# Kernel tuning notes

Measured on AMD Instinct MI355X. Metric: run time of the kernel, lower is better.

The kernel has to match this reference:

```python
import jax, jax.numpy as jnp
import numpy as np

B, H, W, C = 32, 64, 64, 64
F = 128
KH = KW = 3
SH = SW = 1
P = KH * KW * C  # flattened patch size = 576


def _glorot(key, shape):
    fan_in = KH * KW * C
    fan_out = KH * KW * F
    limit = np.sqrt(6.0 / (fan_in + fan_out)).astype(np.float32)
    return jax.random.uniform(key, shape, jnp.float32, -limit, limit)


def setup_inputs() -> dict:
    key = jax.random.key(0)
    k1, k2, k3 = jax.random.split(key, 3)
    inputs = jax.random.normal(k1, (B, H, W, C), dtype=jnp.float32)
    kernel = _glorot(k2, (KH, KW, C, F))
    control_points = _glorot(k3, (KH, KW, C, F))
    bias = jnp.zeros((F,), dtype=jnp.float32)
    return {"inputs": inputs, "kernel": kernel, "bias": bias, "control_points": control_points}


def _extract_patches(x):
    # SAME padding, stride 1; TF extract_patches ordering: (kh, kw, C), C fastest
    xp = jnp.pad(x, ((0, 0), (1, 1), (1, 1), (0, 0)))
    patches = jnp.stack(
        [xp[:, i:i + H, j:j + W, :] for i in range(KH) for j in range(KW)],
        axis=3,
    )  # [B, H, W, KH*KW, C]
    return patches.reshape(B, H, W, P)


def reference(inputs, kernel, bias, control_points):
    conv_out = jax.lax.conv_general_dilated(
        inputs, kernel, (SH, SW), "SAME",
        dimension_numbers=("NHWC", "HWIO", "NHWC"),
    )  # [B, H, W, F]

    # RBF branch via ||a-b||^2 = ||a||^2 + ||b||^2 - 2 a.b
    p = _extract_patches(inputs).reshape(-1, P)        # [N, P]
    c = control_points.reshape(P, F)                   # [P, F]
    pn = jnp.sum(p * p, axis=1, keepdims=True)         # [N, 1]
    cn = jnp.sum(c * c, axis=0)                        # [F]
    d = pn + cn - 2.0 * (p @ c)                        # [N, F] squared distances
    gamma = 1.0 / (2.0 * jnp.mean(d))                  # global mean over all patches/filters
    kan = jnp.exp(-gamma * d).reshape(B, H, W, F)

    return conv_out + kan + bias
```

## Files before the change

kernel.cpp:

```cpp
#include <hip/hip_runtime.h>


#define B_ 32
#define H_ 64
#define W_ 64
#define C_ 64
#define F_ 128
#define P_ 576
#define NPIX (B_*H_*W_)
#define NF   (NPIX*F_)

typedef __bf16  bf16x8 __attribute__((ext_vector_type(8)));
typedef float   f32x4  __attribute__((ext_vector_type(4)));

union BFU { __bf16 h; ushort s; };
union PKU { __bf16 h[2]; uint u; };

__device__ __forceinline__ ushort f2bf(float f) { BFU q; q.h = (__bf16)f; return q.s; }
__device__ __forceinline__ uint pk(float a, float b) {
    PKU q; q.h[0] = (__bf16)a; q.h[1] = (__bf16)b; return q.u;
}

__global__ void k_prep(const float* __restrict__ wgt, const float* __restrict__ ctrl,
                       ushort* __restrict__ wsB, float* __restrict__ cn,
                       float* __restrict__ accum, float* __restrict__ tab) {
    __shared__ __attribute__((aligned(16))) float sh[1024];
    const int t = threadIdx.x;

    if (blockIdx.x < 288) {
        int e = blockIdx.x * 256 + t;
        int p = e >> 7, f = e & 127;
        int kc = p >> 6, r = p & 63;
        int ks = r >> 5, quad = (r >> 3) & 3, j = r & 7;
        int ntg = f >> 4, l16 = f & 15;
        int off0 = (kc * 2 + ks) * 8192 + ntg * 512 + (quad * 16 + l16) * 8 + j;
        wsB[off0]        = f2bf(wgt[e]);
        wsB[off0 + 4096] = f2bf(ctrl[e]);
        return;
    }
    if (blockIdx.x == 288) {
        int col = t & 31, pc8 = t >> 5;
        f32x4 a = {0.f, 0.f, 0.f, 0.f};
        const float* base = ctrl + col * 4;
        #pragma unroll 4
        for (int p = pc8 * 72; p < pc8 * 72 + 72; ++p) {
            f32x4 v = *(const f32x4*)(base + p * F_);
            a += v * v;
        }
        f32x4* sh4 = (f32x4*)sh;
        sh4[t] = a;
        __syncthreads();
        f32x4 s = {0.f, 0.f, 0.f, 0.f};
        if (t < 32) {
            #pragma unroll
            for (int q = 0; q < 8; ++q) s += sh4[q * 32 + t];
            *(f32x4*)(cn + t * 4) = s;
        }
        float tot = s.x + s.y + s.z + s.w;
        if (t < 64) {
            #pragma unroll
            for (int off = 32; off >= 1; off >>= 1) tot += __shfl_down(tot, off, 64);
            if (t == 0) accum[0] = tot;
        }
        return;
    }

    for (int e = t; e < 576; e += 256) {
        const f32x4* row = (const f32x4*)(ctrl + e * F_);
        f32x4 a = {0.f, 0.f, 0.f, 0.f};
        #pragma unroll 8
        for (int q = 0; q < 32; ++q) a += row[q];
        sh[e] = a.x + a.y + a.z + a.w;
    }
    __syncthreads();
    for (int idx = t; idx < 576; idx += 256) {
        int q = idx >> 6, c = idx & 63;
        int ry = q / 3, rx = q - 3 * ry;
        int my = (ry == 0) ? 3 : (ry == 2) ? 6 : 7;
        int mx = (rx == 0) ? 3 : (rx == 2) ? 6 : 7;
        float s = 0.f;
        #pragma unroll
        for (int ki = 0; ki < 3; ++ki)
            #pragma unroll
            for (int kj = 0; kj < 3; ++kj)
                if ((my >> ki & 1) && (mx >> kj & 1))
                    s += sh[(ki * 3 + kj) * 64 + c];
        tab[idx] = s;
    }
}

__launch_bounds__(256)
__global__ void k_gamma(const float* __restrict__ in, const float* __restrict__ tab,
                        float* __restrict__ spn, float* __restrict__ spc) {
    __shared__ float shs[4], shp[4];
    const int t = threadIdx.x, seg = t & 15, grp = t >> 4;
    float s = 0.f, pc = 0.f;
    #pragma unroll 4
    for (int it = 0; it < 16; ++it) {
        int pix = blockIdx.x * 256 + it * 16 + grp;
        int y = (pix >> 6) & 63, x = pix & 63;
        float4 v = *((const float4*)(in + pix * 64) + seg);
        int ry = (y == 0) ? 0 : (y == 63) ? 2 : 1;
        int rx = (x == 0) ? 0 : (x == 63) ? 2 : 1;
        float4 tv = *((const float4*)(tab + (ry * 3 + rx) * 64) + seg);
        float wq = (float)((3 - (y == 0) - (y == 63)) * (3 - (x == 0) - (x == 63)));
        s  += wq * (v.x*v.x + v.y*v.y + v.z*v.z + v.w*v.w);
        pc += v.x*tv.x + v.y*tv.y + v.z*tv.z + v.w*tv.w;
    }
    #pragma unroll
    for (int off = 32; off >= 1; off >>= 1) {
        s  += __shfl_down(s,  off, 64);
        pc += __shfl_down(pc, off, 64);
    }
    if ((t & 63) == 0) { shs[t >> 6] = s; shp[t >> 6] = pc; }
    __syncthreads();
    if (t == 0)  spn[blockIdx.x] = shs[0] + shs[1] + shs[2] + shs[3];
    if (t == 64) spc[blockIdx.x] = shp[0] + shp[1] + shp[2] + shp[3];
}

__launch_bounds__(512, 4)
__global__ void k_main(const float* __restrict__ in, const ushort* __restrict__ wsB,
                       const float* __restrict__ bias, const float* __restrict__ cn,
                       const float* __restrict__ accum, const float* __restrict__ spn,
                       const float* __restrict__ spc, float* __restrict__ out) {
    __shared__ __attribute__((aligned(16))) ushort smem[18208];
    ushort* lI   = smem;
    float*  sArr = (float*)(smem + 17408);
    float*  pnAr = (float*)(smem + 17952);

    const int tid = threadIdx.x;
    const int n0  = blockIdx.x * 128;
    const int b   = n0 >> 12;
    const int y0  = (n0 >> 6) & 63;
    const float* inb = in + b * 262144;

    const int w     = tid >> 6, lane = tid & 63;
    const int fq    = w & 3, mhalf = w >> 2;
    const int quad  = lane >> 4, l16 = lane & 15;
    const int fq2   = fq * 2;

    const uint4* bp = (const uint4*)wsB + fq2 * 64 + lane;

    uint4 cw0 = bp[0],   cw1 = bp[64];
    uint4 cc0 = bp[512], cc1 = bp[576];

    for (int g = tid; g < 2176; g += 512) {
        int row4 = g / 544;
        int rem  = g - row4 * 544;
        int px = rem >> 3, c = rem & 7;
        int y = y0 + row4 - 1, x = px - 1;
        float4 v0 = make_float4(0.f, 0.f, 0.f, 0.f), v1 = v0;
        if (y >= 0 && y < 64 && x >= 0 && x < 64) {
            const float* sp = inb + y * 4096 + x * 64 + c * 8;
            v0 = *(const float4*)sp;
            v1 = *(const float4*)(sp + 4);
        }
        uint4 o = { pk(v0.x, v0.y), pk(v0.z, v0.w), pk(v1.x, v1.y), pk(v1.z, v1.w) };
        *(uint4*)&lI[(row4 * 68 + px) * 64 + ((c ^ (px & 7)) << 3)] = o;
        float s8 = v0.x*v0.x + v0.y*v0.y + v0.z*v0.z + v0.w*v0.w
                 + v1.x*v1.x + v1.y*v1.y + v1.z*v1.z + v1.w*v1.w;
        s8 += __shfl_xor(s8, 1, 64);
        s8 += __shfl_xor(s8, 2, 64);
        s8 += __shfl_xor(s8, 4, 64);
        if ((g & 7) == 0) sArr[row4 * 68 + px] = s8;
    }
    __syncthreads();

    if (tid < 128) {
        int yr = tid >> 6, x = tid & 63;
        float a = 0.f;
        #pragma unroll
        for (int dr = 0; dr < 3; ++dr)
            #pragma unroll
            for (int dc = 0; dc < 3; ++dc)
                a += sArr[(yr + dr) * 68 + x + dc];
        pnAr[tid] = a;
    }
    __syncthreads();

    f32x4 accW[4][2], accC[4][2];
    #pragma unroll
    for (int mt = 0; mt < 4; ++mt)
        #pragma unroll
        for (int nt = 0; nt < 2; ++nt) {
            accW[mt][nt] = (f32x4){0.f, 0.f, 0.f, 0.f};
            accC[mt][nt] = (f32x4){0.f, 0.f, 0.f, 0.f};
        }

    #pragma unroll 1
    for (int t18 = 0; t18 < 18; ++t18) {
        const int kc = t18 >> 1, ks = t18 & 1;
        const int ki = (kc >= 6) ? 2 : (kc >= 3) ? 1 : 0;
        const int kj = kc - 3 * ki;

        uint4 nw0, nw1, nc0, nc1;
        if (t18 < 17) {
            const uint4* np = bp + (t18 + 1) * 1024;
            nw0 = np[0];   nw1 = np[64];
            nc0 = np[512]; nc1 = np[576];
        }

        bf16x8 bw[2], bc[2];
        bw[0] = __builtin_bit_cast(bf16x8, cw0);
        bw[1] = __builtin_bit_cast(bf16x8, cw1);
        bc[0] = __builtin_bit_cast(bf16x8, cc0);
        bc[1] = __builtin_bit_cast(bf16x8, cc1);

        const int swk = (l16 + kj) & 7;
        const int rb0 = (mhalf + ki) * 68 + l16 + kj;
        const int sw  = ((ks * 4 + quad) ^ swk) << 3;
        #pragma unroll
        for (int mt = 0; mt < 4; ++mt) {
            bf16x8 a = *(const bf16x8*)&lI[(rb0 + mt * 16) * 64 + sw];
            #pragma unroll
            for (int nt = 0; nt < 2; ++nt) {
                accW[mt][nt] = __builtin_amdgcn_mfma_f32_16x16x32_bf16(a, bw[nt], accW[mt][nt], 0, 0, 0);
                accC[mt][nt] = __builtin_amdgcn_mfma_f32_16x16x32_bf16(a, bc[nt], accC[mt][nt], 0, 0, 0);
            }
        }
        cw0 = nw0; cw1 = nw1; cc0 = nc0; cc1 = nc1;
    }

    float sp = 0.f, sc = 0.f;
    #pragma unroll
    for (int q = 0; q < 8; ++q) {
        sp += spn[q * 64 + lane];
        sc += spc[q * 64 + lane];
    }
    #pragma unroll
    for (int off = 32; off >= 1; off >>= 1) {
        sp += __shfl_xor(sp, off, 64);
        sc += __shfl_xor(sc, off, 64);
    }
    float Sd = 128.f * sp + 131072.f * accum[0] - 2.f * sc;
    float g  = 0.5f * 16777216.f / Sd;
    float bv[2], cv[2];
    #pragma unroll
    for (int nt = 0; nt < 2; ++nt) {
        int gf = fq * 32 + nt * 16 + l16;
        bv[nt] = bias[gf];
        cv[nt] = cn[gf];
    }
    #pragma unroll
    for (int mt = 0; mt < 4; ++mt) {
        int rloc = mhalf * 64 + mt * 16 + quad * 4;
        float pv[4];
        #pragma unroll
        for (int r = 0; r < 4; ++r) pv[r] = pnAr[rloc + r];
        int gm = n0 + rloc;
        #pragma unroll
        for (int nt = 0; nt < 2; ++nt) {
            int gf = fq * 32 + nt * 16 + l16;
            #pragma unroll
            for (int r = 0; r < 4; ++r) {
                float d = pv[r] + cv[nt] - 2.f * accC[mt][nt][r];
                out[(gm + r) * F_ + gf] = accW[mt][nt][r] + bv[nt] + __expf(-g * d);
            }
        }
    }
}

extern "C" void kernel_launch(void* const* d_in, const int* in_sizes, int n_in,
                              void* d_out, int out_size, void* d_ws, size_t ws_size,
                              hipStream_t stream) {
    const float* in   = (const float*)d_in[0];
    const float* wgt  = (const float*)d_in[1];
    const float* bias = (const float*)d_in[2];
    const float* ctrl = (const float*)d_in[3];
    float* out = (float*)d_out;

    char* ws = (char*)d_ws;
    ushort* wsB   = (ushort*)(ws + 0);
    float*  cn    = (float*) (ws + 294912);
    float*  accum = (float*) (ws + 295424);
    float*  tab   = (float*) (ws + 295488);
    float*  spn   = (float*) (ws + 297792);
    float*  spc   = (float*) (ws + 299840);

    k_prep  <<<290,        256, 0, stream>>>(wgt, ctrl, wsB, cn, accum, tab);
    k_gamma <<<NPIX / 256, 256, 0, stream>>>(in, tab, spn, spc);
    k_main  <<<NPIX / 128, 512, 0, stream>>>(in, wsB, bias, cn, accum, spn, spc, out);
}
```

Before: 142.2 us.

## Shrink main tile to one image row and merge gamma reduction into prep

Each main-kernel block now handles one image row (64 pixels) with 256 threads instead of two rows with 512. This doubles the grid and cuts LDS per block, but also lowers halo reuse, since 3 input rows are loaded per output row instead of 4 per 2. The per-pixel gamma partial-sum work moves into the prep kernel's extra blocks, and the control-point table becomes its own tiny single-block kernel. The launch count stays at three, but the gamma reduction now runs concurrently with weight packing.

New measurement: 151.6 us. 1.07x slower.

```diff
diff --git a/kernel.cpp b/kernel.cpp
--- a/kernel.cpp
+++ b/kernel.cpp
@@ -21,10 +21,40 @@
     PKU q; q.h[0] = (__bf16)a; q.h[1] = (__bf16)b; return q.u;
 }
 
-__global__ void k_prep(const float* __restrict__ wgt, const float* __restrict__ ctrl,
+__global__ void k_tab(const float* __restrict__ ctrl, float* __restrict__ tab) {
+    __shared__ float sh[576];
+    const int t = threadIdx.x;
+    for (int e = t; e < 576; e += 256) {
+        const f32x4* row = (const f32x4*)(ctrl + e * F_);
+        f32x4 a = {0.f, 0.f, 0.f, 0.f};
+        #pragma unroll 8
+        for (int q = 0; q < 32; ++q) a += row[q];
+        sh[e] = a.x + a.y + a.z + a.w;
+    }
+    __syncthreads();
+    for (int idx = t; idx < 576; idx += 256) {
+        int q = idx >> 6, c = idx & 63;
+        int ry = q / 3, rx = q - 3 * ry;
+        int my = (ry == 0) ? 3 : (ry == 2) ? 6 : 7;
+        int mx = (rx == 0) ? 3 : (rx == 2) ? 6 : 7;
+        float s = 0.f;
+        #pragma unroll
+        for (int ki = 0; ki < 3; ++ki)
+            #pragma unroll
+            for (int kj = 0; kj < 3; ++kj)
+                if ((my >> ki & 1) && (mx >> kj & 1))
+                    s += sh[(ki * 3 + kj) * 64 + c];
+        tab[idx] = s;
+    }
+}
+
+__global__ void k_prep(const float* __restrict__ in, const float* __restrict__ wgt,
+                       const float* __restrict__ ctrl, const float* __restrict__ tab,
                        ushort* __restrict__ wsB, float* __restrict__ cn,
-                       float* __restrict__ accum, float* __restrict__ tab) {
+                       float* __restrict__ accum, float* __restrict__ spn,
+                       float* __restrict__ spc) {
     __shared__ __attribute__((aligned(16))) float sh[1024];
+    __shared__ float shs[4], shp[4];
     const int t = threadIdx.x;
 
     if (blockIdx.x < 288) {
@@ -65,39 +95,12 @@
         return;
     }
 
-    for (int e = t; e < 576; e += 256) {
-        const f32x4* row = (const f32x4*)(ctrl + e * F_);
-        f32x4 a = {0.f, 0.f, 0.f, 0.f};
-        #pragma unroll 8
-        for (int q = 0; q < 32; ++q) a += row[q];
-        sh[e] = a.x + a.y + a.z + a.w;
-    }
-    __syncthreads();
-    for (int idx = t; idx < 576; idx += 256) {
-        int q = idx >> 6, c = idx & 63;
-        int ry = q / 3, rx = q - 3 * ry;
-        int my = (ry == 0) ? 3 : (ry == 2) ? 6 : 7;
-        int mx = (rx == 0) ? 3 : (rx == 2) ? 6 : 7;
-        float s = 0.f;
-        #pragma unroll
-        for (int ki = 0; ki < 3; ++ki)
-            #pragma unroll
-            for (int kj = 0; kj < 3; ++kj)
-                if ((my >> ki & 1) && (mx >> kj & 1))
-                    s += sh[(ki * 3 + kj) * 64 + c];
-        tab[idx] = s;
-    }
-}
-
-__launch_bounds__(256)
-__global__ void k_gamma(const float* __restrict__ in, const float* __restrict__ tab,
-                        float* __restrict__ spn, float* __restrict__ spc) {
-    __shared__ float shs[4], shp[4];
-    const int t = threadIdx.x, seg = t & 15, grp = t >> 4;
+    const int sb = blockIdx.x - 289;
+    const int seg = t & 15, grp = t >> 4;
     float s = 0.f, pc = 0.f;
     #pragma unroll 4
     for (int it = 0; it < 16; ++it) {
-        int pix = blockIdx.x * 256 + it * 16 + grp;
+        int pix = sb * 256 + it * 16 + grp;
         int y = (pix >> 6) & 63, x = pix & 63;
         float4 v = *((const float4*)(in + pix * 64) + seg);
         int ry = (y == 0) ? 0 : (y == 63) ? 2 : 1;
@@ -114,28 +117,27 @@
     }
     if ((t & 63) == 0) { shs[t >> 6] = s; shp[t >> 6] = pc; }
     __syncthreads();
-    if (t == 0)  spn[blockIdx.x] = shs[0] + shs[1] + shs[2] + shs[3];
-    if (t == 64) spc[blockIdx.x] = shp[0] + shp[1] + shp[2] + shp[3];
-}
-
-__launch_bounds__(512, 4)
+    if (t == 0)  spn[sb] = shs[0] + shs[1] + shs[2] + shs[3];
+    if (t == 64) spc[sb] = shp[0] + shp[1] + shp[2] + shp[3];
+}
+
+__launch_bounds__(256, 4)
 __global__ void k_main(const float* __restrict__ in, const ushort* __restrict__ wsB,
                        const float* __restrict__ bias, const float* __restrict__ cn,
                        const float* __restrict__ accum, const float* __restrict__ spn,
                        const float* __restrict__ spc, float* __restrict__ out) {
-    __shared__ __attribute__((aligned(16))) ushort smem[18208];
+    __shared__ __attribute__((aligned(16))) ushort smem[13600];
     ushort* lI   = smem;
-    float*  sArr = (float*)(smem + 17408);
-    float*  pnAr = (float*)(smem + 17952);
+    float*  sArr = (float*)(smem + 13056);
+    float*  pnAr = (float*)(smem + 13464);
 
     const int tid = threadIdx.x;
-    const int n0  = blockIdx.x * 128;
+    const int n0  = blockIdx.x * 64;
     const int b   = n0 >> 12;
     const int y0  = (n0 >> 6) & 63;
     const float* inb = in + b * 262144;
 
-    const int w     = tid >> 6, lane = tid & 63;
-    const int fq    = w & 3, mhalf = w >> 2;
+    const int fq    = tid >> 6, lane = tid & 63;
     const int quad  = lane >> 4, l16 = lane & 15;
     const int fq2   = fq * 2;
 
@@ -144,11 +146,11 @@
     uint4 cw0 = bp[0],   cw1 = bp[64];
     uint4 cc0 = bp[512], cc1 = bp[576];
 
-    for (int g = tid; g < 2176; g += 512) {
-        int row4 = g / 544;
-        int rem  = g - row4 * 544;
+    for (int g = tid; g < 1632; g += 256) {
+        int row3 = g / 544;
+        int rem  = g - row3 * 544;
         int px = rem >> 3, c = rem & 7;
-        int y = y0 + row4 - 1, x = px - 1;
+        int y = y0 + row3 - 1, x = px - 1;
         float4 v0 = make_float4(0.f, 0.f, 0.f, 0.f), v1 = v0;
         if (y >= 0 && y < 64 && x >= 0 && x < 64) {
             const float* sp = inb + y * 4096 + x * 64 + c * 8;
@@ -156,24 +158,23 @@
             v1 = *(const float4*)(sp + 4);
         }
         uint4 o = { pk(v0.x, v0.y), pk(v0.z, v0.w), pk(v1.x, v1.y), pk(v1.z, v1.w) };
-        *(uint4*)&lI[(row4 * 68 + px) * 64 + ((c ^ (px & 7)) << 3)] = o;
+        *(uint4*)&lI[(row3 * 68 + px) * 64 + ((c ^ (px & 7)) << 3)] = o;
         float s8 = v0.x*v0.x + v0.y*v0.y + v0.z*v0.z + v0.w*v0.w
                  + v1.x*v1.x + v1.y*v1.y + v1.z*v1.z + v1.w*v1.w;
         s8 += __shfl_xor(s8, 1, 64);
         s8 += __shfl_xor(s8, 2, 64);
         s8 += __shfl_xor(s8, 4, 64);
-        if ((g & 7) == 0) sArr[row4 * 68 + px] = s8;
-    }
-    __syncthreads();
-
-    if (tid < 128) {
-        int yr = tid >> 6, x = tid & 63;
+        if ((g & 7) == 0) sArr[row3 * 68 + px] = s8;
+    }
+    __syncthreads();
+
+    if (tid < 64) {
         float a = 0.f;
         #pragma unroll
         for (int dr = 0; dr < 3; ++dr)
             #pragma unroll
             for (int dc = 0; dc < 3; ++dc)
-                a += sArr[(yr + dr) * 68 + x + dc];
+                a += sArr[dr * 68 + tid + dc];
         pnAr[tid] = a;
     }
     __syncthreads();
@@ -207,7 +208,7 @@
         bc[1] = __builtin_bit_cast(bf16x8, cc1);
 
         const int swk = (l16 + kj) & 7;
-        const int rb0 = (mhalf + ki) * 68 + l16 + kj;
+        const int rb0 = ki * 68 + l16 + kj;
         const int sw  = ((ks * 4 + quad) ^ swk) << 3;
         #pragma unroll
         for (int mt = 0; mt < 4; ++mt) {
@@ -243,7 +244,7 @@
     }
     #pragma unroll
     for (int mt = 0; mt < 4; ++mt) {
-        int rloc = mhalf * 64 + mt * 16 + quad * 4;
+        int rloc = mt * 16 + quad * 4;
         float pv[4];
         #pragma unroll
         for (int r = 0; r < 4; ++r) pv[r] = pnAr[rloc + r];
@@ -277,7 +278,7 @@
     float*  spn   = (float*) (ws + 297792);
     float*  spc   = (float*) (ws + 299840);
 
-    k_prep  <<<290,        256, 0, stream>>>(wgt, ctrl, wsB, cn, accum, tab);
-    k_gamma <<<NPIX / 256, 256, 0, stream>>>(in, tab, spn, spc);
-    k_main  <<<NPIX / 128, 512, 0, stream>>>(in, wsB, bias, cn, accum, spn, spc, out);
-}
+    k_tab  <<<1,         256, 0, stream>>>(ctrl, tab);
+    k_prep <<<801,       256, 0, stream>>>(in, wgt, ctrl, tab, wsB, cn, accum, spn, spc);
+    k_main <<<NPIX / 64, 256, 0, stream>>>(in, wsB, bias, cn, accum, spn, spc, out);
+}
```

## Pre-convert input to padded swizzled bf16 image and stage via global_load_lds

Applied to the files above, without the earlier changes.

k_gamma now also writes a bf16, row-padded, XOR-swizzled copy of the input plus per-pixel squared norms into workspace. k_main loads its halo tile straight into LDS with global_load_lds, skipping per-block fp32 loads, conversion and duplicate halo reads. Patch norms come from a 3x3 box sum of the per-pixel norms. This adds an extra 17 MB write/read pass through the workspace, and a fallback kernel covers the case where the workspace is too small.

Result: slower. 153.9 us (+8.2%).

```diff
diff --git a/kernel.cpp b/kernel.cpp
--- a/kernel.cpp
+++ b/kernel.cpp
@@ -21,9 +21,15 @@
     PKU q; q.h[0] = (__bf16)a; q.h[1] = (__bf16)b; return q.u;
 }
 
+__device__ __forceinline__ void gll16(const void* g, void* l) {
+    __builtin_amdgcn_global_load_lds((const __attribute__((address_space(1))) void*)g,
+                                     (__attribute__((address_space(3))) void*)l, 16, 0, 0);
+}
+
 __global__ void k_prep(const float* __restrict__ wgt, const float* __restrict__ ctrl,
                        ushort* __restrict__ wsB, float* __restrict__ cn,
-                       float* __restrict__ accum, float* __restrict__ tab) {
+                       float* __restrict__ accum, float* __restrict__ tab,
+                       uint4* __restrict__ zeroblk) {
     __shared__ __attribute__((aligned(16))) float sh[1024];
     const int t = threadIdx.x;
 
@@ -39,6 +45,7 @@
         return;
     }
     if (blockIdx.x == 288) {
+        if (t < 8) zeroblk[t] = (uint4){0u, 0u, 0u, 0u};
         int col = t & 31, pc8 = t >> 5;
         f32x4 a = {0.f, 0.f, 0.f, 0.f};
         const float* base = ctrl + col * 4;
@@ -91,9 +98,12 @@
 
 __launch_bounds__(256)
 __global__ void k_gamma(const float* __restrict__ in, const float* __restrict__ tab,
-                        float* __restrict__ spn, float* __restrict__ spc) {
+                        float* __restrict__ spn, float* __restrict__ spc,
+                        ushort* __restrict__ imgbf, float* __restrict__ sG,
+                        int wimg) {
     __shared__ float shs[4], shp[4];
     const int t = threadIdx.x, seg = t & 15, grp = t >> 4;
+    const int cc = seg >> 1, half = seg & 1;
     float s = 0.f, pc = 0.f;
     #pragma unroll 4
     for (int it = 0; it < 16; ++it) {
@@ -104,8 +114,28 @@
         int rx = (x == 0) ? 0 : (x == 63) ? 2 : 1;
         float4 tv = *((const float4*)(tab + (ry * 3 + rx) * 64) + seg);
         float wq = (float)((3 - (y == 0) - (y == 63)) * (3 - (x == 0) - (x == 63)));
-        s  += wq * (v.x*v.x + v.y*v.y + v.z*v.z + v.w*v.w);
+        float s4 = v.x*v.x + v.y*v.y + v.z*v.z + v.w*v.w;
+        s  += wq * s4;
         pc += v.x*tv.x + v.y*tv.y + v.z*tv.z + v.w*tv.w;
+        if (wimg) {
+            int px = x + 1;
+            ushort* dst = imgbf + (size_t)(pix >> 6) * 4352 + px * 64
+                        + ((cc ^ (px & 7)) << 3) + (half << 2);
+            uint2 o = { pk(v.x, v.y), pk(v.z, v.w) };
+            *(uint2*)dst = o;
+            float ss = s4;
+            ss += __shfl_xor(ss, 1, 64);
+            ss += __shfl_xor(ss, 2, 64);
+            ss += __shfl_xor(ss, 4, 64);
+            ss += __shfl_xor(ss, 8, 64);
+            if (seg == 0) sG[pix] = ss;
+        }
+    }
+    if (wimg && t < 128) {
+        int r = t >> 5, hp = (t >> 3) & 3, q = t & 7;
+        int px = (hp == 0) ? 0 : (64 + hp);
+        ushort* dst = imgbf + (size_t)(blockIdx.x * 4 + r) * 4352 + px * 64 + q * 8;
+        *(uint4*)dst = (uint4){0u, 0u, 0u, 0u};
     }
     #pragma unroll
     for (int off = 32; off >= 1; off >>= 1) {
@@ -119,10 +149,150 @@
 }
 
 __launch_bounds__(512, 4)
-__global__ void k_main(const float* __restrict__ in, const ushort* __restrict__ wsB,
+__global__ void k_main(const ushort* __restrict__ imgbf, const float* __restrict__ sG,
+                       const uint4* __restrict__ zeroblk, const ushort* __restrict__ wsB,
                        const float* __restrict__ bias, const float* __restrict__ cn,
                        const float* __restrict__ accum, const float* __restrict__ spn,
                        const float* __restrict__ spc, float* __restrict__ out) {
+    __shared__ __attribute__((aligned(16))) ushort smem[17664];
+    ushort* lI   = smem;
+    float*  pnAr = (float*)(smem + 17408);
+
+    const int tid = threadIdx.x;
+    const int n0  = blockIdx.x * 128;
+    const int b   = n0 >> 12;
+    const int y0  = (n0 >> 6) & 63;
+
+    const int w     = tid >> 6, lane = tid & 63;
+    const int fq    = w & 3, mhalf = w >> 2;
+    const int quad  = lane >> 4, l16 = lane & 15;
+    const int fq2   = fq * 2;
+
+    const uint4* bp = (const uint4*)wsB + fq2 * 64 + lane;
+
+    uint4 cw0 = bp[0],   cw1 = bp[64];
+    uint4 cc0 = bp[512], cc1 = bp[576];
+
+    #pragma unroll
+    for (int i = 0; i < 5; ++i) {
+        int g = tid + i * 512;
+        if (i < 4 || tid < 128) {
+            int row4 = g / 544;
+            int rem  = g - row4 * 544;
+            int yy   = y0 + row4 - 1;
+            const char* src = (yy >= 0 && yy < 64)
+                ? (const char*)(imgbf + (size_t)(b * 64 + yy) * 4352 + rem * 8)
+                : (const char*)zeroblk;
+            gll16(src, (char*)lI + g * 16);
+        }
+    }
+
+    if (tid < 128) {
+        int yr = tid >> 6, x = tid & 63;
+        int y = y0 + yr;
+        float a = 0.f;
+        #pragma unroll
+        for (int dy = -1; dy <= 1; ++dy) {
+            int yy = y + dy;
+            if (yy < 0 || yy > 63) continue;
+            const float* sr = sG + ((b * 64 + yy) << 6);
+            #pragma unroll
+            for (int dx = -1; dx <= 1; ++dx) {
+                int xx = x + dx;
+                if (xx >= 0 && xx <= 63) a += sr[xx];
+            }
+        }
+        pnAr[tid] = a;
+    }
+    __syncthreads();
+
+    f32x4 accW[4][2], accC[4][2];
+    #pragma unroll
+    for (int mt = 0; mt < 4; ++mt)
+        #pragma unroll
+        for (int nt = 0; nt < 2; ++nt) {
+            accW[mt][nt] = (f32x4){0.f, 0.f, 0.f, 0.f};
+            accC[mt][nt] = (f32x4){0.f, 0.f, 0.f, 0.f};
+        }
+
+    #pragma unroll 1
+    for (int t18 = 0; t18 < 18; ++t18) {
+        const int kc = t18 >> 1, ks = t18 & 1;
+        const int ki = (kc >= 6) ? 2 : (kc >= 3) ? 1 : 0;
+        const int kj = kc - 3 * ki;
+
+        uint4 nw0, nw1, nc0, nc1;
+        if (t18 < 17) {
+            const uint4* np = bp + (t18 + 1) * 1024;
+            nw0 = np[0];   nw1 = np[64];
+            nc0 = np[512]; nc1 = np[576];
+        }
+
+        bf16x8 bw[2], bc[2];
+        bw[0] = __builtin_bit_cast(bf16x8, cw0);
+        bw[1] = __builtin_bit_cast(bf16x8, cw1);
+        bc[0] = __builtin_bit_cast(bf16x8, cc0);
+        bc[1] = __builtin_bit_cast(bf16x8, cc1);
+
+        const int swk = (l16 + kj) & 7;
+        const int rb0 = (mhalf + ki) * 68 + l16 + kj;
+        const int sw  = ((ks * 4 + quad) ^ swk) << 3;
+        #pragma unroll
+        for (int mt = 0; mt < 4; ++mt) {
+            bf16x8 a = *(const bf16x8*)&lI[(rb0 + mt * 16) * 64 + sw];
+            #pragma unroll
+            for (int nt = 0; nt < 2; ++nt) {
+                accW[mt][nt] = __builtin_amdgcn_mfma_f32_16x16x32_bf16(a, bw[nt], accW[mt][nt], 0, 0, 0);
+                accC[mt][nt] = __builtin_amdgcn_mfma_f32_16x16x32_bf16(a, bc[nt], accC[mt][nt], 0, 0, 0);
+            }
+        }
+        cw0 = nw0; cw1 = nw1; cc0 = nc0; cc1 = nc1;
+    }
+
+    float sp = 0.f, sc = 0.f;
+    #pragma unroll
+    for (int q = 0; q < 8; ++q) {
+        sp += spn[q * 64 + lane];
+        sc += spc[q * 64 + lane];
+    }
+    #pragma unroll
+    for (int off = 32; off >= 1; off >>= 1) {
+        sp += __shfl_xor(sp, off, 64);
+        sc += __shfl_xor(sc, off, 64);
+    }
+    float Sd = 128.f * sp + 131072.f * accum[0] - 2.f * sc;
+    float g  = 0.5f * 16777216.f / Sd;
+    float bv[2], cv[2];
+    #pragma unroll
+    for (int nt = 0; nt < 2; ++nt) {
+        int gf = fq * 32 + nt * 16 + l16;
+        bv[nt] = bias[gf];
+        cv[nt] = cn[gf];
+    }
+    #pragma unroll
+    for (int mt = 0; mt < 4; ++mt) {
+        int rloc = mhalf * 64 + mt * 16 + quad * 4;
+        float pv[4];
+        #pragma unroll
+        for (int r = 0; r < 4; ++r) pv[r] = pnAr[rloc + r];
+        int gm = n0 + rloc;
+        #pragma unroll
+        for (int nt = 0; nt < 2; ++nt) {
+            int gf = fq * 32 + nt * 16 + l16;
+            #pragma unroll
+            for (int r = 0; r < 4; ++r) {
+                float d = pv[r] + cv[nt] - 2.f * accC[mt][nt][r];
+                out[(gm + r) * F_ + gf] = accW[mt][nt][r] + bv[nt] + __expf(-g * d);
+            }
+        }
+    }
+}
+
+__launch_bounds__(512, 4)
+__global__ void k_main_fb(const float* __restrict__ in, const ushort* __restrict__ wsB,
+                          const float* __restrict__ bias, const float* __restrict__ cn,
+                          const float* __restrict__ accum, const float* __restrict__ spn,
+                          const float* __restrict__ spc, float* __restrict__ out) {
     __shared__ __attribute__((aligned(16))) ushort smem[18208];
     ushort* lI   = smem;
     float*  sArr = (float*)(smem + 17408);
@@ -140,7 +310,6 @@
     const int fq2   = fq * 2;
 
     const uint4* bp = (const uint4*)wsB + fq2 * 64 + lane;
-
     uint4 cw0 = bp[0],   cw1 = bp[64];
     uint4 cc0 = bp[512], cc1 = bp[576];
 
@@ -270,14 +439,22 @@
     float* out = (float*)d_out;
 
     char* ws = (char*)d_ws;
-    ushort* wsB   = (ushort*)(ws + 0);
-    float*  cn    = (float*) (ws + 294912);
-    float*  accum = (float*) (ws + 295424);
-    float*  tab   = (float*) (ws + 295488);
-    float*  spn   = (float*) (ws + 297792);
-    float*  spc   = (float*) (ws + 299840);
-
-    k_prep  <<<290,        256, 0, stream>>>(wgt, ctrl, wsB, cn, accum, tab);
-    k_gamma <<<NPIX / 256, 256, 0, stream>>>(in, tab, spn, spc);
-    k_main  <<<NPIX / 128, 512, 0, stream>>>(in, wsB, bias, cn, accum, spn, spc, out);
-}
+    ushort* wsB    = (ushort*)(ws + 0);
+    float*  cn     = (float*) (ws + 294912);
+    float*  accum  = (float*) (ws + 295424);
+    float*  tab    = (float*) (ws + 295488);
+    float*  spn    = (float*) (ws + 297792);
+    float*  spc    = (float*) (ws + 299840);
+    uint4*  zeroblk= (uint4*) (ws + 301888);
+    float*  sG     = (float*) (ws + 302080);
+    ushort* imgbf  = (ushort*)(ws + 826368);
+    const int fast = (ws_size >= (size_t)(826368 + 17825792)) ? 1 : 0;
+
+    k_prep  <<<290,        256, 0, stream>>>(wgt, ctrl, wsB, cn, accum, tab, zeroblk);
+    k_gamma <<<NPIX / 256, 256, 0, stream>>>(in, tab, spn, spc, imgbf, sG, fast);
+    if (fast)
+        k_main    <<<NPIX / 128, 512, 0, stream>>>(imgbf, sG, zeroblk, wsB, bias, cn,
+                                                   accum, spn, spc, out);
+    else
+        k_main_fb <<<NPIX / 128, 512, 0, stream>>>(in, wsB, bias, cn, accum, spn, spc, out);
+}
```

## Switch main GEMM to 32x32x16 MFMA tiles with matching weight layout

Applied to the files above, without the earlier changes.

Replaces the 16x16x32 bf16 MFMA tiling (4x2 fragments per wave) with 32x32x16 MFMA (2 M-tiles by 1 N-tile per wave), and reorders the pre-swizzled weight buffer to match the new B-fragment layout. The aim is fewer LDS A-fragment reads per FLOP and fewer MFMA issues, since the larger instruction carries more work per operand load. The epilogue is rewritten for the 32x32 accumulator row mapping. The A-row index expression contains an odd term multiplied by zero, and the changed LDS swizzle and access pattern could introduce bank conflicts.

Measured after the change: 148.6 us. 4.5% more time.

```diff
diff --git a/kernel.cpp b/kernel.cpp
--- a/kernel.cpp
+++ b/kernel.cpp
@@ -10,8 +10,9 @@
 #define NPIX (B_*H_*W_)
 #define NF   (NPIX*F_)
 
-typedef __bf16  bf16x8 __attribute__((ext_vector_type(8)));
-typedef float   f32x4  __attribute__((ext_vector_type(4)));
+typedef __bf16  bf16x8  __attribute__((ext_vector_type(8)));
+typedef float   f32x4   __attribute__((ext_vector_type(4)));
+typedef float   f32x16  __attribute__((ext_vector_type(16)));
 
 union BFU { __bf16 h; ushort s; };
 union PKU { __bf16 h[2]; uint u; };
@@ -30,12 +31,10 @@
     if (blockIdx.x < 288) {
         int e = blockIdx.x * 256 + t;
         int p = e >> 7, f = e & 127;
-        int kc = p >> 6, r = p & 63;
-        int ks = r >> 5, quad = (r >> 3) & 3, j = r & 7;
-        int ntg = f >> 4, l16 = f & 15;
-        int off0 = (kc * 2 + ks) * 8192 + ntg * 512 + (quad * 16 + l16) * 8 + j;
+        int off0 = (((p >> 4) * 2) * 4 + (f >> 5)) * 512
+                 + ((p >> 3) & 1) * 256 + (f & 31) * 8 + (p & 7);
         wsB[off0]        = f2bf(wgt[e]);
-        wsB[off0 + 4096] = f2bf(ctrl[e]);
+        wsB[off0 + 2048] = f2bf(ctrl[e]);
         return;
     }
     if (blockIdx.x == 288) {
@@ -136,13 +135,12 @@
 
     const int w     = tid >> 6, lane = tid & 63;
     const int fq    = w & 3, mhalf = w >> 2;
-    const int quad  = lane >> 4, l16 = lane & 15;
-    const int fq2   = fq * 2;
-
-    const uint4* bp = (const uint4*)wsB + fq2 * 64 + lane;
-
-    uint4 cw0 = bp[0],   cw1 = bp[64];
-    uint4 cc0 = bp[512], cc1 = bp[576];
+    const int l31   = lane & 31, hi = lane >> 5;
+
+    const uint4* bp = (const uint4*)wsB + fq * 64 + lane;
+
+    uint4 cw0 = bp[0],   cc0 = bp[256];
+    uint4 cw1 = bp[512], cc1 = bp[768];
 
     for (int g = tid; g < 2176; g += 512) {
         int row4 = g / 544;
@@ -178,47 +176,44 @@
     }
     __syncthreads();
 
-    f32x4 accW[4][2], accC[4][2];
-    #pragma unroll
-    for (int mt = 0; mt < 4; ++mt)
-        #pragma unroll
-        for (int nt = 0; nt < 2; ++nt) {
-            accW[mt][nt] = (f32x4){0.f, 0.f, 0.f, 0.f};
-            accC[mt][nt] = (f32x4){0.f, 0.f, 0.f, 0.f};
-        }
+    f32x16 accW[2], accC[2];
+    #pragma unroll
+    for (int mt = 0; mt < 2; ++mt) {
+        accW[mt] = (f32x16){0.f};
+        accC[mt] = (f32x16){0.f};
+    }
 
     #pragma unroll 1
-    for (int t18 = 0; t18 < 18; ++t18) {
-        const int kc = t18 >> 1, ks = t18 & 1;
+    for (int i = 0; i < 18; ++i) {
+        const int kc = i >> 1, ks32 = i & 1;
         const int ki = (kc >= 6) ? 2 : (kc >= 3) ? 1 : 0;
         const int kj = kc - 3 * ki;
 
-        uint4 nw0, nw1, nc0, nc1;
-        if (t18 < 17) {
-            const uint4* np = bp + (t18 + 1) * 1024;
-            nw0 = np[0];   nw1 = np[64];
-            nc0 = np[512]; nc1 = np[576];
-        }
-
-        bf16x8 bw[2], bc[2];
-        bw[0] = __builtin_bit_cast(bf16x8, cw0);
-        bw[1] = __builtin_bit_cast(bf16x8, cw1);
-        bc[0] = __builtin_bit_cast(bf16x8, cc0);
-        bc[1] = __builtin_bit_cast(bf16x8, cc1);
-
-        const int swk = (l16 + kj) & 7;
-        const int rb0 = (mhalf + ki) * 68 + l16 + kj;
-        const int sw  = ((ks * 4 + quad) ^ swk) << 3;
-        #pragma unroll
-        for (int mt = 0; mt < 4; ++mt) {
-            bf16x8 a = *(const bf16x8*)&lI[(rb0 + mt * 16) * 64 + sw];
-            #pragma unroll
-            for (int nt = 0; nt < 2; ++nt) {
-                accW[mt][nt] = __builtin_amdgcn_mfma_f32_16x16x32_bf16(a, bw[nt], accW[mt][nt], 0, 0, 0);
-                accC[mt][nt] = __builtin_amdgcn_mfma_f32_16x16x32_bf16(a, bc[nt], accC[mt][nt], 0, 0, 0);
-            }
-        }
-        cw0 = nw0; cw1 = nw1; cc0 = nc0; cc1 = nc1;
+        uint4 nw0, nc0, nw1, nc1;
+        if (i < 17) {
+            const uint4* np = bp + (i + 1) * 1024;
+            nw0 = np[0];   nc0 = np[256];
+            nw1 = np[512]; nc1 = np[768];
+        }
+
+        const int px  = l31 + kj;
+        const int swk = px & 7;
+        const int rb0 = (mhalf + ki) * 68 + px;
+        const int cb  = ks32 * 4 + hi;
+
+        #pragma unroll
+        for (int ks16 = 0; ks16 < 2; ++ks16) {
+            const int slot = ((cb + ks16 * 2) ^ swk) << 3;
+            bf16x8 a0 = *(const bf16x8*)&lI[rb0 * 64 + slot];
+            bf16x8 a1 = *(const bf16x8*)&lI[(rb0 + 32 * 68 / 68 * 2048 / 64 + 0) * 0 + (rb0 + 32) * 64 + slot];
+            bf16x8 bw = __builtin_bit_cast(bf16x8, ks16 ? cw1 : cw0);
+            bf16x8 bc = __builtin_bit_cast(bf16x8, ks16 ? cc1 : cc0);
+            accW[0] = __builtin_amdgcn_mfma_f32_32x32x16_bf16(a0, bw, accW[0], 0, 0, 0);
+            accW[1] = __builtin_amdgcn_mfma_f32_32x32x16_bf16(a1, bw, accW[1], 0, 0, 0);
+            accC[0] = __builtin_amdgcn_mfma_f32_32x32x16_bf16(a0, bc, accC[0], 0, 0, 0);
+            accC[1] = __builtin_amdgcn_mfma_f32_32x32x16_bf16(a1, bc, accC[1], 0, 0, 0);
+        }
+        cw0 = nw0; cc0 = nc0; cw1 = nw1; cc1 = nc1;
     }
 
     float sp = 0.f, sc = 0.f;
@@ -234,28 +229,18 @@
     }
     float Sd = 128.f * sp + 131072.f * accum[0] - 2.f * sc;
     float g  = 0.5f * 16777216.f / Sd;
-    float bv[2], cv[2];
-    #pragma unroll
-    for (int nt = 0; nt < 2; ++nt) {
-        int gf = fq * 32 + nt * 16 + l16;
-        bv[nt] = bias[gf];
-        cv[nt] = cn[gf];
-    }
-    #pragma unroll
-    for (int mt = 0; mt < 4; ++mt) {
-        int rloc = mhalf * 64 + mt * 16 + quad * 4;
-        float pv[4];
-        #pragma unroll
-        for (int r = 0; r < 4; ++r) pv[r] = pnAr[rloc + r];
-        int gm = n0 + rloc;
-        #pragma unroll
-        for (int nt = 0; nt < 2; ++nt) {
-            int gf = fq * 32 + nt * 16 + l16;
-            #pragma unroll
-            for (int r = 0; r < 4; ++r) {
-                float d = pv[r] + cv[nt] - 2.f * accC[mt][nt][r];
-                out[(gm + r) * F_ + gf] = accW[mt][nt][r] + bv[nt] + __expf(-g * d);
-            }
+    const int gf = fq * 32 + l31;
+    const float bv = bias[gf];
+    const float cv = cn[gf];
+    #pragma unroll
+    for (int mt = 0; mt < 2; ++mt) {
+        #pragma unroll
+        for (int r = 0; r < 16; ++r) {
+            int rowfrag = (r & 3) + 8 * (r >> 2) + 4 * hi;
+            int rloc = mhalf * 64 + mt * 32 + rowfrag;
+            float pv = pnAr[rloc];
+            float d  = pv + cv - 2.f * accC[mt][r];
+            out[(n0 + rloc) * F_ + gf] = accW[mt][r] + bv + __expf(-g * d);
         }
     }
 }
```
